# Kernel optimization log

Hardware: AMD Instinct MI355X
Metric: run time of the kernel (lower is better)

## Reference

```python
import jax, jax.numpy as jnp
import numpy as np

N = 50000      # nodes (single node type 'mapping_var')
IN = 128       # in_feats
HID = 128      # hid_feats
OUT = 64       # out_feats
R = 3          # number of relations
E = 800000     # edges per relation (avg degree 16)
NEG_SLOPE = 0.01  # F.leaky_relu default


def setup_inputs() -> dict:
    key = jax.random.key(0)
    ks = jax.random.split(key, 9)
    s = 0.05
    return {
        "x": jax.random.normal(ks[0], (N, IN), jnp.float32),
        "edge_src": jax.random.randint(ks[1], (R, E), 0, N, jnp.int32),
        "edge_dst": jax.random.randint(ks[2], (R, E), 0, N, jnp.int32),
        "W0": jax.random.normal(ks[3], (R, IN, HID), jnp.float32) * s,
        "b0": jnp.zeros((R, HID), jnp.float32),
        "Wl": jax.random.normal(ks[4], (4, R, HID, HID), jnp.float32) * s,
        "bl": jnp.zeros((4, R, HID), jnp.float32),
        "Wout": jax.random.normal(ks[5], (HID, OUT), jnp.float32) * s,
        "bout": jnp.zeros((OUT,), jnp.float32),
    }


def _hetero_conv(h, edge_src, edge_dst, W, b):
    """One HeteroGraphConv layer: per-relation GraphConv (norm='both') then
    mean-aggregate across relations.  h: [N, Din], W: [R, Din, Dout]."""
    ones = jnp.ones((E,), h.dtype)
    outs = []
    for r in range(R):
        src, dst = edge_src[r], edge_dst[r]
        out_deg = jax.ops.segment_sum(ones, src, num_segments=N)
        in_deg = jax.ops.segment_sum(ones, dst, num_segments=N)
        # src-side normalization D_out^{-1/2}
        hn = h * jax.lax.rsqrt(jnp.maximum(out_deg, 1.0))[:, None]
        # gather messages along edges, sum into destinations
        agg = jax.ops.segment_sum(hn[src], dst, num_segments=N)
        # dst-side normalization D_in^{-1/2}
        agg = agg * jax.lax.rsqrt(jnp.maximum(in_deg, 1.0))[:, None]
        outs.append(agg @ W[r] + b[r])
    return jnp.mean(jnp.stack(outs, axis=0), axis=0)  # 'mean' cross-relation aggregate


def reference(x, edge_src, edge_dst, W0, b0, Wl, bl, Wout, bout):
    # Layer 0: in_feats -> hid_feats
    h = _hetero_conv(x, edge_src, edge_dst, W0, b0)
    h = jax.nn.leaky_relu(h, NEG_SLOPE)  # dropout omitted (eval mode)
    # Layers 1..4: hid -> hid; activation after all but the last
    for l in range(4):
        h = _hetero_conv(h, edge_src, edge_dst, Wl[l], bl[l])
        if l != 3:
            h = jax.nn.leaky_relu(h, NEG_SLOPE)
    # final Linear on h['mapping_var']
    return h @ Wout + bout
```

## Files before the change

### kernel.cpp

```cpp
#include <hip/hip_runtime.h>
#include <hip/hip_bf16.h>
#include <cstddef>
#include <cstdint>

#define NNODES 50000
#define NR 3
#define NE 800000
#define HIDF 128
#define OUTF 64
#define NEG_SLOPE 0.01f
#define SCAN_T 1024
#define NCHUNK ((NNODES + SCAN_T - 1) / SCAN_T)
#define KTOT (NR * HIDF)
#define KU (KTOT / 2)
#define RN (NR * NNODES)

__device__ __forceinline__ float bf_lo(uint v) { return __uint_as_float(v << 16); }
__device__ __forceinline__ float bf_hi(uint v) { return __uint_as_float(v & 0xffff0000u); }
__device__ __forceinline__ uint bf_rne(float f) {
    uint u = __float_as_uint(f);
    return (u + 0x7fffu + ((u >> 16) & 1u)) >> 16;
}
__device__ __forceinline__ uint bf_pack(float a, float b) {
    return bf_rne(a) | (bf_rne(b) << 16);
}

typedef short bf16x8 __attribute__((ext_vector_type(8)));
typedef float f32x4 __attribute__((ext_vector_type(4)));
__device__ __forceinline__ bf16x8 as_bf(uint4 v) { return __builtin_bit_cast(bf16x8, v); }

__global__ __launch_bounds__(256) void k_cast_x(const float* __restrict__ x,
                                                uint* __restrict__ xb) {
    int i = blockIdx.x * blockDim.x + threadIdx.x;
    if (i >= NNODES * (HIDF / 2)) return;
    float2 v = *(const float2*)(x + (size_t)i * 2);
    xb[i] = bf_pack(v.x, v.y);
}

__global__ __launch_bounds__(256) void k_cast_w(const float* __restrict__ W0,
                                                const float* __restrict__ Wl,
                                                uint* __restrict__ wbT) {
    int idx = blockIdx.x * blockDim.x + threadIdx.x;
    if (idx >= 5 * HIDF * KU) return;
    int l = idx / (HIDF * KU);
    int rem = idx - l * (HIDF * KU);
    int t = rem / HIDF;
    int n = rem - t * HIDF;
    int r = t / 64;
    int kk = (t - r * 64) * 2;
    const float* Wsrc = (l == 0) ? W0 : Wl + (size_t)(l - 1) * NR * HIDF * HIDF;
    const float* wp = Wsrc + ((size_t)r * HIDF + kk) * HIDF + n;
    float a = wp[0];
    float b = wp[HIDF];
    wbT[(size_t)l * HIDF * KU + (size_t)n * KU + t] = bf_pack(a, b);
}

__global__ __launch_bounds__(256) void k_count(const int* __restrict__ esrc,
                                               const int* __restrict__ edst,
                                               int* __restrict__ deg_out,
                                               int* __restrict__ deg_in,
                                               ushort* __restrict__ epos) {
    int idx = blockIdx.x * blockDim.x + threadIdx.x;
    if (idx >= NR * NE) return;
    int r = idx / NE;
    int s = esrc[idx];
    int d = edst[idx];
    atomicAdd(&deg_out[r * NNODES + s], 1);
    int p = atomicAdd(&deg_in[r * NNODES + d], 1);
    epos[idx] = (ushort)p;
}

__global__ __launch_bounds__(256) void k_norms(const int* __restrict__ deg_out,
                                               const int* __restrict__ deg_in,
                                               float* __restrict__ out_norm,
                                               float* __restrict__ in_norm) {
    int idx = blockIdx.x * blockDim.x + threadIdx.x;
    if (idx >= RN) return;
    int dout = deg_out[idx];
    int din  = deg_in[idx];
    out_norm[idx] = rsqrtf((float)(dout > 1 ? dout : 1));
    in_norm[idx]  = rsqrtf((float)(din  > 1 ? din  : 1));
}

__global__ __launch_bounds__(SCAN_T) void k_scan1(const int* __restrict__ deg_in,
                                                  int* __restrict__ row_ptr,
                                                  int* __restrict__ csums) {
    __shared__ int buf[SCAN_T];
    int r = blockIdx.x / NCHUNK;
    int c = blockIdx.x % NCHUNK;
    int tid = threadIdx.x;
    int i = c * SCAN_T + tid;
    int v = (i < NNODES) ? deg_in[r * NNODES + i] : 0;
    buf[tid] = v;
    __syncthreads();
    for (int off = 1; off < SCAN_T; off <<= 1) {
        int t = (tid >= off) ? buf[tid - off] : 0;
        __syncthreads();
        buf[tid] += t;
        __syncthreads();
    }
    if (i < NNODES) row_ptr[r * (NNODES + 1) + i + 1] = buf[tid];
    if (tid == SCAN_T - 1) csums[r * NCHUNK + c] = buf[SCAN_T - 1];
}

__global__ void k_scan2(const int* __restrict__ csums, int* __restrict__ coffs) {
    int r = threadIdx.x;
    if (r >= NR) return;
    int run = 0;
    for (int c = 0; c < NCHUNK; ++c) {
        coffs[r * NCHUNK + c] = run;
        run += csums[r * NCHUNK + c];
    }
}

__global__ __launch_bounds__(SCAN_T) void k_scan3(int* __restrict__ row_ptr,
                                                  const int* __restrict__ coffs) {
    int r = blockIdx.x / NCHUNK;
    int c = blockIdx.x % NCHUNK;
    int tid = threadIdx.x;
    int i = c * SCAN_T + tid;
    int off = coffs[r * NCHUNK + c];
    if (i < NNODES) row_ptr[r * (NNODES + 1) + i + 1] += off;
    if (tid == 0 && c == 0) row_ptr[r * (NNODES + 1)] = 0;
}

__global__ __launch_bounds__(256) void k_fill_csr(const int* __restrict__ esrc,
                                                  const int* __restrict__ edst,
                                                  const int* __restrict__ row_ptr,
                                                  const ushort* __restrict__ epos,
                                                  const float* __restrict__ out_norm,
                                                  int2* __restrict__ csr_sw) {
    int idx = blockIdx.x * blockDim.x + threadIdx.x;
    if (idx >= NR * NE) return;
    int r = idx / NE;
    int s = esrc[idx];
    int d = edst[idx];
    float w = out_norm[r * NNODES + s];
    int slot = row_ptr[r * (NNODES + 1) + d] + (int)epos[idx];
    csr_sw[(size_t)r * NE + slot] = make_int2(s, __float_as_int(w));
}

__global__ __launch_bounds__(256) void k_aggregate(const uint* __restrict__ hin,
                                                   const float* __restrict__ in_norm,
                                                   const int* __restrict__ row_ptr,
                                                   const int2* __restrict__ csr_sw,
                                                   uint* __restrict__ aggb) {
    int wave = blockIdx.x * 4 + (threadIdx.x >> 6);
    if (wave >= RN) return;
    int r = wave / NNODES;
    int n = wave - r * NNODES;
    int lane = threadIdx.x & 63;
    int quarter = lane >> 4;
    int sub = lane & 15;
    int start = row_ptr[r * (NNODES + 1) + n];
    int end   = row_ptr[r * (NNODES + 1) + n + 1];
    const int2* cw = csr_sw + (size_t)r * NE;

    float acc[8];
#pragma unroll
    for (int k = 0; k < 8; ++k) acc[k] = 0.f;

    int i = start;
    int last = end - 1;
    for (; i + 8 <= end; i += 8) {
        int2 eA = cw[i + quarter];
        int2 eB = cw[i + 4 + quarter];
        uint4 vA = *(const uint4*)(hin + (size_t)eA.x * (HIDF / 2) + sub * 4);
        uint4 vB = *(const uint4*)(hin + (size_t)eB.x * (HIDF / 2) + sub * 4);
        float wA = __int_as_float(eA.y);
        float wB = __int_as_float(eB.y);
        acc[0] = fmaf(wA, bf_lo(vA.x), acc[0]); acc[1] = fmaf(wA, bf_hi(vA.x), acc[1]);
        acc[2] = fmaf(wA, bf_lo(vA.y), acc[2]); acc[3] = fmaf(wA, bf_hi(vA.y), acc[3]);
        acc[4] = fmaf(wA, bf_lo(vA.z), acc[4]); acc[5] = fmaf(wA, bf_hi(vA.z), acc[5]);
        acc[6] = fmaf(wA, bf_lo(vA.w), acc[6]); acc[7] = fmaf(wA, bf_hi(vA.w), acc[7]);
        acc[0] = fmaf(wB, bf_lo(vB.x), acc[0]); acc[1] = fmaf(wB, bf_hi(vB.x), acc[1]);
        acc[2] = fmaf(wB, bf_lo(vB.y), acc[2]); acc[3] = fmaf(wB, bf_hi(vB.y), acc[3]);
        acc[4] = fmaf(wB, bf_lo(vB.z), acc[4]); acc[5] = fmaf(wB, bf_hi(vB.z), acc[5]);
        acc[6] = fmaf(wB, bf_lo(vB.w), acc[6]); acc[7] = fmaf(wB, bf_hi(vB.w), acc[7]);
    }
    for (; i < end; i += 4) {
        int e_idx = i + quarter;
        bool act = e_idx < end;
        int2 e = cw[act ? e_idx : last];
        float w = act ? __int_as_float(e.y) : 0.f;
        uint4 v = *(const uint4*)(hin + (size_t)e.x * (HIDF / 2) + sub * 4);
        acc[0] = fmaf(w, bf_lo(v.x), acc[0]); acc[1] = fmaf(w, bf_hi(v.x), acc[1]);
        acc[2] = fmaf(w, bf_lo(v.y), acc[2]); acc[3] = fmaf(w, bf_hi(v.y), acc[3]);
        acc[4] = fmaf(w, bf_lo(v.z), acc[4]); acc[5] = fmaf(w, bf_hi(v.z), acc[5]);
        acc[6] = fmaf(w, bf_lo(v.w), acc[6]); acc[7] = fmaf(w, bf_hi(v.w), acc[7]);
    }

#pragma unroll
    for (int k = 0; k < 8; ++k) {
        acc[k] += __shfl_xor(acc[k], 16);
        acc[k] += __shfl_xor(acc[k], 32);
    }

    if (quarter == 0) {
        float wn = in_norm[r * NNODES + n];
        uint4 pk;
        pk.x = bf_pack(acc[0] * wn, acc[1] * wn);
        pk.y = bf_pack(acc[2] * wn, acc[3] * wn);
        pk.z = bf_pack(acc[4] * wn, acc[5] * wn);
        pk.w = bf_pack(acc[6] * wn, acc[7] * wn);
        *(uint4*)(aggb + (size_t)n * KU + r * (HIDF / 2) + sub * 4) = pk;
    }
}

__global__ __launch_bounds__(256) void k_conv_mm(const uint* __restrict__ aggb,
                                                 const uint* __restrict__ wbT,
                                                 const float* __restrict__ bias,
                                                 ushort* __restrict__ hout,
                                                 int act) {
    int wv   = threadIdx.x >> 6;
    int lane = threadIdx.x & 63;
    int lrow = lane & 15;
    int kgrp = lane >> 4;
    int rb = blockIdx.x * 128 + wv * 32;

    f32x4 acc[2][8];
#pragma unroll
    for (int m = 0; m < 2; ++m)
#pragma unroll
        for (int nr = 0; nr < 8; ++nr) acc[m][nr] = (f32x4){0.f, 0.f, 0.f, 0.f};

    int row0 = rb + lrow;
    int row1 = rb + 16 + lrow;
    bool v0 = row0 < NNODES;
    bool v1 = row1 < NNODES;
    const uint* a0p = aggb + (size_t)row0 * KU + kgrp * 4;
    const uint* a1p = aggb + (size_t)row1 * KU + kgrp * 4;
    const uint* bp  = wbT + (size_t)lrow * KU + kgrp * 4;
    const uint4 za = make_uint4(0u, 0u, 0u, 0u);

#pragma unroll
    for (int ks = 0; ks < KTOT / 32; ++ks) {
        uint4 ua0 = v0 ? *(const uint4*)(a0p + ks * 16) : za;
        uint4 ua1 = v1 ? *(const uint4*)(a1p + ks * 16) : za;
        bf16x8 af0 = as_bf(ua0);
        bf16x8 af1 = as_bf(ua1);
#pragma unroll
        for (int nr = 0; nr < 8; ++nr) {
            uint4 ub = *(const uint4*)(bp + (size_t)nr * (16 * KU) + ks * 16);
            bf16x8 bf = as_bf(ub);
            acc[0][nr] = __builtin_amdgcn_mfma_f32_16x16x32_bf16(af0, bf, acc[0][nr], 0, 0, 0);
            acc[1][nr] = __builtin_amdgcn_mfma_f32_16x16x32_bf16(af1, bf, acc[1][nr], 0, 0, 0);
        }
    }

    const float inv3 = 1.f / 3.f;
#pragma unroll
    for (int nr = 0; nr < 8; ++nr) {
        int col = nr * 16 + lrow;
        float bm = (bias[col] + bias[HIDF + col] + bias[2 * HIDF + col]) * inv3;
#pragma unroll
        for (int m = 0; m < 2; ++m) {
            int rbase = rb + m * 16 + kgrp * 4;
#pragma unroll
            for (int i = 0; i < 4; ++i) {
                int row = rbase + i;
                if (row >= NNODES) continue;
                float t = acc[m][nr][i] * inv3 + bm;
                if (act) t = (t > 0.f) ? t : NEG_SLOPE * t;
                hout[(size_t)row * HIDF + col] = (ushort)bf_rne(t);
            }
        }
    }
}

__global__ __launch_bounds__(256) void k_final(const uint* __restrict__ h,
                                               const float* __restrict__ Wout,
                                               const float* __restrict__ bout,
                                               float* __restrict__ out) {
    int tid = threadIdx.x;
    int col = tid & 63;
    int row = blockIdx.x * 4 + (tid >> 6);
    if (row >= NNODES) return;
    const uint* hp = h + (size_t)row * (HIDF / 2);
    float acc = bout[col];
#pragma unroll 8
    for (int ku = 0; ku < HIDF / 2; ++ku) {
        uint v = hp[ku];
        acc = fmaf(bf_lo(v), Wout[(2 * ku) * OUTF + col], acc);
        acc = fmaf(bf_hi(v), Wout[(2 * ku + 1) * OUTF + col], acc);
    }
    out[(size_t)row * OUTF + col] = acc;
}

extern "C" void kernel_launch(void* const* d_in, const int* in_sizes, int n_in,
                              void* d_out, int out_size, void* d_ws, size_t ws_size,
                              hipStream_t stream) {
    const float* x    = (const float*)d_in[0];
    const int*   esrc = (const int*)d_in[1];
    const int*   edst = (const int*)d_in[2];
    const float* W0   = (const float*)d_in[3];
    const float* b0   = (const float*)d_in[4];
    const float* Wl   = (const float*)d_in[5];
    const float* bl   = (const float*)d_in[6];
    const float* Wout = (const float*)d_in[7];
    const float* bout = (const float*)d_in[8];
    float* out = (float*)d_out;

    char* ws = (char*)d_ws;
    size_t off = 0;
    auto carve = [&](size_t bytes) {
        size_t p = off;
        off += (bytes + 255) & ~(size_t)255;
        return p;
    };
    const size_t SZ_RN_I = (size_t)RN * 4;
    size_t o_deg_out = carve(SZ_RN_I);
    size_t o_deg_in  = carve(SZ_RN_I);
    size_t zero_span = off;
    size_t o_out_nrm = carve(SZ_RN_I);
    size_t o_in_nrm  = carve(SZ_RN_I);
    size_t o_row_ptr = carve((size_t)NR * (NNODES + 1) * 4);
    size_t o_csums   = carve((size_t)NR * NCHUNK * 4);
    size_t o_coffs   = carve((size_t)NR * NCHUNK * 4);
    size_t o_csr     = carve((size_t)NR * NE * 8);
    size_t o_epos    = carve((size_t)NR * NE * 2);
    size_t o_aggb    = carve((size_t)NNODES * KU * 4);
    size_t o_xb      = carve((size_t)NNODES * (HIDF / 2) * 4);
    size_t o_h       = carve((size_t)NNODES * (HIDF / 2) * 4);
    size_t o_wbT     = carve((size_t)5 * HIDF * KU * 4);
    (void)ws_size;

    int*    deg_out  = (int*)(ws + o_deg_out);
    int*    deg_in   = (int*)(ws + o_deg_in);
    float*  out_norm = (float*)(ws + o_out_nrm);
    float*  in_norm  = (float*)(ws + o_in_nrm);
    int*    row_ptr  = (int*)(ws + o_row_ptr);
    int*    csums    = (int*)(ws + o_csums);
    int*    coffs    = (int*)(ws + o_coffs);
    int2*   csr_sw   = (int2*)(ws + o_csr);
    ushort* epos     = (ushort*)(ws + o_epos);
    uint*   aggb     = (uint*)(ws + o_aggb);
    uint*   xb       = (uint*)(ws + o_xb);
    uint*   h        = (uint*)(ws + o_h);
    uint*   wbT      = (uint*)(ws + o_wbT);

    hipMemsetAsync(ws, 0, zero_span, stream);

    int nEdgeBlocks = (NR * NE + 255) / 256;
    k_cast_x<<<(NNODES * (HIDF / 2) + 255) / 256, 256, 0, stream>>>(x, xb);
    k_cast_w<<<(5 * HIDF * KU + 255) / 256, 256, 0, stream>>>(W0, Wl, wbT);
    k_count<<<nEdgeBlocks, 256, 0, stream>>>(esrc, edst, deg_out, deg_in, epos);
    k_norms<<<(RN + 255) / 256, 256, 0, stream>>>(deg_out, deg_in, out_norm, in_norm);
    k_scan1<<<NR * NCHUNK, SCAN_T, 0, stream>>>(deg_in, row_ptr, csums);
    k_scan2<<<1, 64, 0, stream>>>(csums, coffs);
    k_scan3<<<NR * NCHUNK, SCAN_T, 0, stream>>>(row_ptr, coffs);
    k_fill_csr<<<nEdgeBlocks, 256, 0, stream>>>(esrc, edst, row_ptr, epos, out_norm, csr_sw);

    const int aggBlocks = (RN + 3) / 4;
    const int mmBlocks  = (NNODES + 127) / 128;

    const uint* hin = xb;
    for (int l = 0; l < 5; ++l) {
        k_aggregate<<<aggBlocks, 256, 0, stream>>>(hin, in_norm, row_ptr, csr_sw, aggb);
        const uint*  Wp = wbT + (size_t)l * HIDF * KU;
        const float* bp = (l == 0) ? b0 : bl + (size_t)(l - 1) * NR * HIDF;
        k_conv_mm<<<mmBlocks, 256, 0, stream>>>(aggb, Wp, bp, (ushort*)h, (l < 4) ? 1 : 0);
        hin = h;
    }
    k_final<<<(NNODES + 3) / 4, 256, 0, stream>>>(h, Wout, bout, out);
}
```

Measured before the change: 1.088 ms.

## Fuse neighbor aggregation and relation matmul into one per-layer kernel

Merges the gather-aggregate kernel and the MFMA projection into a single kernel per layer. Each block aggregates 32 nodes across all three relations into a shared-memory tile, then runs the bf16 MFMA against the stacked weights and writes the activated output. This drops the global round trip of the aggregated buffer, and ping-pong output buffers are added so the fused kernel never reads and writes the same array. The gather loop is also unrolled to 16 edges for more memory-level parallelism, at the cost of fewer blocks, more registers, and weight loads repeated per 32-row block.

```diff
diff --git a/kernel.cpp b/kernel.cpp
--- a/kernel.cpp
+++ b/kernel.cpp
@@ -14,6 +14,8 @@
 #define KTOT (NR * HIDF)
 #define KU (KTOT / 2)
 #define RN (NR * NNODES)
+#define TROW 32
+#define LPAD 196
 
 __device__ __forceinline__ float bf_lo(uint v) { return __uint_as_float(v << 16); }
 __device__ __forceinline__ float bf_hi(uint v) { return __uint_as_float(v & 0xffff0000u); }
@@ -140,130 +142,144 @@
     csr_sw[(size_t)r * NE + slot] = make_int2(s, __float_as_int(w));
 }
 
-__global__ __launch_bounds__(256) void k_aggregate(const uint* __restrict__ hin,
-                                                   const float* __restrict__ in_norm,
-                                                   const int* __restrict__ row_ptr,
-                                                   const int2* __restrict__ csr_sw,
-                                                   uint* __restrict__ aggb) {
-    int wave = blockIdx.x * 4 + (threadIdx.x >> 6);
-    if (wave >= RN) return;
-    int r = wave / NNODES;
-    int n = wave - r * NNODES;
+__global__ __launch_bounds__(256) void k_layer(const uint* __restrict__ hin,
+                                               const float* __restrict__ in_norm,
+                                               const int* __restrict__ row_ptr,
+                                               const int2* __restrict__ csr_sw,
+                                               const uint* __restrict__ wbT,
+                                               const float* __restrict__ bias,
+                                               ushort* __restrict__ hout,
+                                               int act) {
+    __shared__ uint At[TROW][LPAD];
+    int w = threadIdx.x >> 6;
     int lane = threadIdx.x & 63;
     int quarter = lane >> 4;
     int sub = lane & 15;
-    int start = row_ptr[r * (NNODES + 1) + n];
-    int end   = row_ptr[r * (NNODES + 1) + n + 1];
-    const int2* cw = csr_sw + (size_t)r * NE;
-
-    float acc[8];
-#pragma unroll
-    for (int k = 0; k < 8; ++k) acc[k] = 0.f;
-
-    int i = start;
-    int last = end - 1;
-    for (; i + 8 <= end; i += 8) {
-        int2 eA = cw[i + quarter];
-        int2 eB = cw[i + 4 + quarter];
-        uint4 vA = *(const uint4*)(hin + (size_t)eA.x * (HIDF / 2) + sub * 4);
-        uint4 vB = *(const uint4*)(hin + (size_t)eB.x * (HIDF / 2) + sub * 4);
-        float wA = __int_as_float(eA.y);
-        float wB = __int_as_float(eB.y);
-        acc[0] = fmaf(wA, bf_lo(vA.x), acc[0]); acc[1] = fmaf(wA, bf_hi(vA.x), acc[1]);
-        acc[2] = fmaf(wA, bf_lo(vA.y), acc[2]); acc[3] = fmaf(wA, bf_hi(vA.y), acc[3]);
-        acc[4] = fmaf(wA, bf_lo(vA.z), acc[4]); acc[5] = fmaf(wA, bf_hi(vA.z), acc[5]);
-        acc[6] = fmaf(wA, bf_lo(vA.w), acc[6]); acc[7] = fmaf(wA, bf_hi(vA.w), acc[7]);
-        acc[0] = fmaf(wB, bf_lo(vB.x), acc[0]); acc[1] = fmaf(wB, bf_hi(vB.x), acc[1]);
-        acc[2] = fmaf(wB, bf_lo(vB.y), acc[2]); acc[3] = fmaf(wB, bf_hi(vB.y), acc[3]);
-        acc[4] = fmaf(wB, bf_lo(vB.z), acc[4]); acc[5] = fmaf(wB, bf_hi(vB.z), acc[5]);
-        acc[6] = fmaf(wB, bf_lo(vB.w), acc[6]); acc[7] = fmaf(wB, bf_hi(vB.w), acc[7]);
-    }
-    for (; i < end; i += 4) {
-        int e_idx = i + quarter;
-        bool act = e_idx < end;
-        int2 e = cw[act ? e_idx : last];
-        float w = act ? __int_as_float(e.y) : 0.f;
-        uint4 v = *(const uint4*)(hin + (size_t)e.x * (HIDF / 2) + sub * 4);
-        acc[0] = fmaf(w, bf_lo(v.x), acc[0]); acc[1] = fmaf(w, bf_hi(v.x), acc[1]);
-        acc[2] = fmaf(w, bf_lo(v.y), acc[2]); acc[3] = fmaf(w, bf_hi(v.y), acc[3]);
-        acc[4] = fmaf(w, bf_lo(v.z), acc[4]); acc[5] = fmaf(w, bf_hi(v.z), acc[5]);
-        acc[6] = fmaf(w, bf_lo(v.w), acc[6]); acc[7] = fmaf(w, bf_hi(v.w), acc[7]);
-    }
-
-#pragma unroll
-    for (int k = 0; k < 8; ++k) {
-        acc[k] += __shfl_xor(acc[k], 16);
-        acc[k] += __shfl_xor(acc[k], 32);
-    }
-
-    if (quarter == 0) {
-        float wn = in_norm[r * NNODES + n];
-        uint4 pk;
-        pk.x = bf_pack(acc[0] * wn, acc[1] * wn);
-        pk.y = bf_pack(acc[2] * wn, acc[3] * wn);
-        pk.z = bf_pack(acc[4] * wn, acc[5] * wn);
-        pk.w = bf_pack(acc[6] * wn, acc[7] * wn);
-        *(uint4*)(aggb + (size_t)n * KU + r * (HIDF / 2) + sub * 4) = pk;
-    }
-}
-
-__global__ __launch_bounds__(256) void k_conv_mm(const uint* __restrict__ aggb,
-                                                 const uint* __restrict__ wbT,
-                                                 const float* __restrict__ bias,
-                                                 ushort* __restrict__ hout,
-                                                 int act) {
-    int wv   = threadIdx.x >> 6;
-    int lane = threadIdx.x & 63;
+    int rb = blockIdx.x * TROW;
+
+    for (int u = w; u < NR * TROW; u += 4) {
+        int r = u >> 5;
+        int lr = u & 31;
+        int n = rb + lr;
+        if (n < NNODES) {
+            int start = row_ptr[r * (NNODES + 1) + n];
+            int end   = row_ptr[r * (NNODES + 1) + n + 1];
+            const int2* cw = csr_sw + (size_t)r * NE;
+            float acc[8];
+#pragma unroll
+            for (int k = 0; k < 8; ++k) acc[k] = 0.f;
+            int i = start;
+            int last = end - 1;
+            for (; i + 16 <= end; i += 16) {
+                int2 e0 = cw[i + quarter];
+                int2 e1 = cw[i + 4 + quarter];
+                int2 e2 = cw[i + 8 + quarter];
+                int2 e3 = cw[i + 12 + quarter];
+                uint4 v0 = *(const uint4*)(hin + (size_t)e0.x * (HIDF / 2) + sub * 4);
+                uint4 v1 = *(const uint4*)(hin + (size_t)e1.x * (HIDF / 2) + sub * 4);
+                uint4 v2 = *(const uint4*)(hin + (size_t)e2.x * (HIDF / 2) + sub * 4);
+                uint4 v3 = *(const uint4*)(hin + (size_t)e3.x * (HIDF / 2) + sub * 4);
+                float w0 = __int_as_float(e0.y);
+                float w1 = __int_as_float(e1.y);
+                float w2 = __int_as_float(e2.y);
+                float w3 = __int_as_float(e3.y);
+                acc[0] = fmaf(w0, bf_lo(v0.x), acc[0]); acc[1] = fmaf(w0, bf_hi(v0.x), acc[1]);
+                acc[2] = fmaf(w0, bf_lo(v0.y), acc[2]); acc[3] = fmaf(w0, bf_hi(v0.y), acc[3]);
+                acc[4] = fmaf(w0, bf_lo(v0.z), acc[4]); acc[5] = fmaf(w0, bf_hi(v0.z), acc[5]);
+                acc[6] = fmaf(w0, bf_lo(v0.w), acc[6]); acc[7] = fmaf(w0, bf_hi(v0.w), acc[7]);
+                acc[0] = fmaf(w1, bf_lo(v1.x), acc[0]); acc[1] = fmaf(w1, bf_hi(v1.x), acc[1]);
+                acc[2] = fmaf(w1, bf_lo(v1.y), acc[2]); acc[3] = fmaf(w1, bf_hi(v1.y), acc[3]);
+                acc[4] = fmaf(w1, bf_lo(v1.z), acc[4]); acc[5] = fmaf(w1, bf_hi(v1.z), acc[5]);
+                acc[6] = fmaf(w1, bf_lo(v1.w), acc[6]); acc[7] = fmaf(w1, bf_hi(v1.w), acc[7]);
+                acc[0] = fmaf(w2, bf_lo(v2.x), acc[0]); acc[1] = fmaf(w2, bf_hi(v2.x), acc[1]);
+                acc[2] = fmaf(w2, bf_lo(v2.y), acc[2]); acc[3] = fmaf(w2, bf_hi(v2.y), acc[3]);
+                acc[4] = fmaf(w2, bf_lo(v2.z), acc[4]); acc[5] = fmaf(w2, bf_hi(v2.z), acc[5]);
+                acc[6] = fmaf(w2, bf_lo(v2.w), acc[6]); acc[7] = fmaf(w2, bf_hi(v2.w), acc[7]);
+                acc[0] = fmaf(w3, bf_lo(v3.x), acc[0]); acc[1] = fmaf(w3, bf_hi(v3.x), acc[1]);
+                acc[2] = fmaf(w3, bf_lo(v3.y), acc[2]); acc[3] = fmaf(w3, bf_hi(v3.y), acc[3]);
+                acc[4] = fmaf(w3, bf_lo(v3.z), acc[4]); acc[5] = fmaf(w3, bf_hi(v3.z), acc[5]);
+                acc[6] = fmaf(w3, bf_lo(v3.w), acc[6]); acc[7] = fmaf(w3, bf_hi(v3.w), acc[7]);
+            }
+            for (; i + 8 <= end; i += 8) {
+                int2 eA = cw[i + quarter];
+                int2 eB = cw[i + 4 + quarter];
+                uint4 vA = *(const uint4*)(hin + (size_t)eA.x * (HIDF / 2) + sub * 4);
+                uint4 vB = *(const uint4*)(hin + (size_t)eB.x * (HIDF / 2) + sub * 4);
+                float wA = __int_as_float(eA.y);
+                float wB = __int_as_float(eB.y);
+                acc[0] = fmaf(wA, bf_lo(vA.x), acc[0]); acc[1] = fmaf(wA, bf_hi(vA.x), acc[1]);
+                acc[2] = fmaf(wA, bf_lo(vA.y), acc[2]); acc[3] = fmaf(wA, bf_hi(vA.y), acc[3]);
+                acc[4] = fmaf(wA, bf_lo(vA.z), acc[4]); acc[5] = fmaf(wA, bf_hi(vA.z), acc[5]);
+                acc[6] = fmaf(wA, bf_lo(vA.w), acc[6]); acc[7] = fmaf(wA, bf_hi(vA.w), acc[7]);
+                acc[0] = fmaf(wB, bf_lo(vB.x), acc[0]); acc[1] = fmaf(wB, bf_hi(vB.x), acc[1]);
+                acc[2] = fmaf(wB, bf_lo(vB.y), acc[2]); acc[3] = fmaf(wB, bf_hi(vB.y), acc[3]);
+                acc[4] = fmaf(wB, bf_lo(vB.z), acc[4]); acc[5] = fmaf(wB, bf_hi(vB.z), acc[5]);
+                acc[6] = fmaf(wB, bf_lo(vB.w), acc[6]); acc[7] = fmaf(wB, bf_hi(vB.w), acc[7]);
+            }
+            for (; i < end; i += 4) {
+                int e_idx = i + quarter;
+                bool live = e_idx < end;
+                int2 e = cw[live ? e_idx : last];
+                float ww = live ? __int_as_float(e.y) : 0.f;
+                uint4 v = *(const uint4*)(hin + (size_t)e.x * (HIDF / 2) + sub * 4);
+                acc[0] = fmaf(ww, bf_lo(v.x), acc[0]); acc[1] = fmaf(ww, bf_hi(v.x), acc[1]);
+                acc[2] = fmaf(ww, bf_lo(v.y), acc[2]); acc[3] = fmaf(ww, bf_hi(v.y), acc[3]);
+                acc[4] = fmaf(ww, bf_lo(v.z), acc[4]); acc[5] = fmaf(ww, bf_hi(v.z), acc[5]);
+                acc[6] = fmaf(ww, bf_lo(v.w), acc[6]); acc[7] = fmaf(ww, bf_hi(v.w), acc[7]);
+            }
+#pragma unroll
+            for (int k = 0; k < 8; ++k) {
+                acc[k] += __shfl_xor(acc[k], 16);
+                acc[k] += __shfl_xor(acc[k], 32);
+            }
+            if (quarter == 0) {
+                float wn = in_norm[r * NNODES + n];
+                uint4 pk;
+                pk.x = bf_pack(acc[0] * wn, acc[1] * wn);
+                pk.y = bf_pack(acc[2] * wn, acc[3] * wn);
+                pk.z = bf_pack(acc[4] * wn, acc[5] * wn);
+                pk.w = bf_pack(acc[6] * wn, acc[7] * wn);
+                *(uint4*)&At[lr][r * 64 + sub * 4] = pk;
+            }
+        } else if (quarter == 0) {
+            *(uint4*)&At[lr][r * 64 + sub * 4] = make_uint4(0u, 0u, 0u, 0u);
+        }
+    }
+    __syncthreads();
+
     int lrow = lane & 15;
     int kgrp = lane >> 4;
-    int rb = blockIdx.x * 128 + wv * 32;
-
-    f32x4 acc[2][8];
-#pragma unroll
-    for (int m = 0; m < 2; ++m)
-#pragma unroll
-        for (int nr = 0; nr < 8; ++nr) acc[m][nr] = (f32x4){0.f, 0.f, 0.f, 0.f};
-
-    int row0 = rb + lrow;
-    int row1 = rb + 16 + lrow;
-    bool v0 = row0 < NNODES;
-    bool v1 = row1 < NNODES;
-    const uint* a0p = aggb + (size_t)row0 * KU + kgrp * 4;
-    const uint* a1p = aggb + (size_t)row1 * KU + kgrp * 4;
-    const uint* bp  = wbT + (size_t)lrow * KU + kgrp * 4;
-    const uint4 za = make_uint4(0u, 0u, 0u, 0u);
-
+    int rowhalf = (w >> 1) * 16;
+    int colhalf = (w & 1) * 64;
+
+    f32x4 acc2[4];
+#pragma unroll
+    for (int nr = 0; nr < 4; ++nr) acc2[nr] = (f32x4){0.f, 0.f, 0.f, 0.f};
+
+    const uint* bp = wbT + (size_t)(colhalf + lrow) * KU + kgrp * 4;
 #pragma unroll
     for (int ks = 0; ks < KTOT / 32; ++ks) {
-        uint4 ua0 = v0 ? *(const uint4*)(a0p + ks * 16) : za;
-        uint4 ua1 = v1 ? *(const uint4*)(a1p + ks * 16) : za;
-        bf16x8 af0 = as_bf(ua0);
-        bf16x8 af1 = as_bf(ua1);
-#pragma unroll
-        for (int nr = 0; nr < 8; ++nr) {
+        bf16x8 af = as_bf(*(const uint4*)&At[rowhalf + lrow][ks * 16 + kgrp * 4]);
+#pragma unroll
+        for (int nr = 0; nr < 4; ++nr) {
             uint4 ub = *(const uint4*)(bp + (size_t)nr * (16 * KU) + ks * 16);
             bf16x8 bf = as_bf(ub);
-            acc[0][nr] = __builtin_amdgcn_mfma_f32_16x16x32_bf16(af0, bf, acc[0][nr], 0, 0, 0);
-            acc[1][nr] = __builtin_amdgcn_mfma_f32_16x16x32_bf16(af1, bf, acc[1][nr], 0, 0, 0);
+            acc2[nr] = __builtin_amdgcn_mfma_f32_16x16x32_bf16(af, bf, acc2[nr], 0, 0, 0);
         }
     }
 
     const float inv3 = 1.f / 3.f;
 #pragma unroll
-    for (int nr = 0; nr < 8; ++nr) {
-        int col = nr * 16 + lrow;
+    for (int nr = 0; nr < 4; ++nr) {
+        int col = colhalf + nr * 16 + lrow;
         float bm = (bias[col] + bias[HIDF + col] + bias[2 * HIDF + col]) * inv3;
 #pragma unroll
-        for (int m = 0; m < 2; ++m) {
-            int rbase = rb + m * 16 + kgrp * 4;
-#pragma unroll
-            for (int i = 0; i < 4; ++i) {
-                int row = rbase + i;
-                if (row >= NNODES) continue;
-                float t = acc[m][nr][i] * inv3 + bm;
-                if (act) t = (t > 0.f) ? t : NEG_SLOPE * t;
-                hout[(size_t)row * HIDF + col] = (ushort)bf_rne(t);
-            }
+        for (int i = 0; i < 4; ++i) {
+            int row = rb + rowhalf + kgrp * 4 + i;
+            if (row >= NNODES) continue;
+            float t = acc2[nr][i] * inv3 + bm;
+            if (act) t = (t > 0.f) ? t : NEG_SLOPE * t;
+            hout[(size_t)row * HIDF + col] = (ushort)bf_rne(t);
         }
     }
 }
@@ -319,9 +335,9 @@
     size_t o_coffs   = carve((size_t)NR * NCHUNK * 4);
     size_t o_csr     = carve((size_t)NR * NE * 8);
     size_t o_epos    = carve((size_t)NR * NE * 2);
-    size_t o_aggb    = carve((size_t)NNODES * KU * 4);
     size_t o_xb      = carve((size_t)NNODES * (HIDF / 2) * 4);
-    size_t o_h       = carve((size_t)NNODES * (HIDF / 2) * 4);
+    size_t o_h0      = carve((size_t)NNODES * (HIDF / 2) * 4);
+    size_t o_h1      = carve((size_t)NNODES * (HIDF / 2) * 4);
     size_t o_wbT     = carve((size_t)5 * HIDF * KU * 4);
     (void)ws_size;
 
@@ -334,9 +350,9 @@
     int*    coffs    = (int*)(ws + o_coffs);
     int2*   csr_sw   = (int2*)(ws + o_csr);
     ushort* epos     = (ushort*)(ws + o_epos);
-    uint*   aggb     = (uint*)(ws + o_aggb);
     uint*   xb       = (uint*)(ws + o_xb);
-    uint*   h        = (uint*)(ws + o_h);
+    uint*   h0       = (uint*)(ws + o_h0);
+    uint*   h1       = (uint*)(ws + o_h1);
     uint*   wbT      = (uint*)(ws + o_wbT);
 
     hipMemsetAsync(ws, 0, zero_span, stream);
@@ -351,16 +367,17 @@
     k_scan3<<<NR * NCHUNK, SCAN_T, 0, stream>>>(row_ptr, coffs);
     k_fill_csr<<<nEdgeBlocks, 256, 0, stream>>>(esrc, edst, row_ptr, epos, out_norm, csr_sw);
 
-    const int aggBlocks = (RN + 3) / 4;
-    const int mmBlocks  = (NNODES + 127) / 128;
-
+    const int layerBlocks = (NNODES + TROW - 1) / TROW;
+
+    uint* bufs[2] = {h0, h1};
     const uint* hin = xb;
     for (int l = 0; l < 5; ++l) {
-        k_aggregate<<<aggBlocks, 256, 0, stream>>>(hin, in_norm, row_ptr, csr_sw, aggb);
+        uint* hout = bufs[l & 1];
         const uint*  Wp = wbT + (size_t)l * HIDF * KU;
         const float* bp = (l == 0) ? b0 : bl + (size_t)(l - 1) * NR * HIDF;
-        k_conv_mm<<<mmBlocks, 256, 0, stream>>>(aggb, Wp, bp, (ushort*)h, (l < 4) ? 1 : 0);
-        hin = h;
-    }
-    k_final<<<(NNODES + 3) / 4, 256, 0, stream>>>(h, Wout, bout, out);
-}
+        k_layer<<<layerBlocks, 256, 0, stream>>>(hin, in_norm, row_ptr, csr_sw, Wp, bp,
+                                                 (ushort*)hout, (l < 4) ? 1 : 0);
+        hin = hout;
+    }
+    k_final<<<(NNODES + 3) / 4, 256, 0, stream>>>(bufs[0], Wout, bout, out);
+}
```

Measured after the change: 1.242 ms. +14.2%, slower.
